# Kernel tuning notes

Hardware: AMD Instinct MI355X
Metric: run time of the kernel (lower is better)

Reference implementation:

```python
import jax, jax.numpy as jnp
import numpy as np

MARGIN = 0.5  # hardcoded in the torch __init__ regardless of the margin arg
P_IDS, K_PER_ID, K_PER_MOD = 32, 8, 4
B, C = P_IDS * K_PER_ID, 1024


def setup_inputs() -> dict:
    key = jax.random.key(0)
    inputs = jax.random.normal(key, (B, C), dtype=jnp.float32)
    # Standard cross-modal ReID sampler: P identities, K instances each,
    # first K/2 from modality 0, last K/2 from modality 1. This guarantees the
    # boolean-mask reshape in the original code is well-formed (M per row).
    targets = jnp.repeat(jnp.arange(P_IDS, dtype=jnp.int32), K_PER_ID)
    subs = jnp.tile(jnp.repeat(jnp.arange(2, dtype=jnp.int32), K_PER_MOD), P_IDS)
    return {"inputs": inputs, "targets": targets, "subs": subs, "m_count": K_PER_MOD}


def _loss(inputs, targets, subs, m_count):
    b, c = inputs.shape
    # Mask construction uses detached inputs in the original (clone().detach()).
    xs = jax.lax.stop_gradient(inputs)
    diff = jnp.abs(xs[:, None, :] - xs[None, :, :])                     # (B,B,C)
    identity_mask = targets[:, None] == targets[None, :]                # (B,B)
    modality_mask = subs[:, None] == subs[None, :]                      # (B,B)
    combined = identity_mask & modality_mask                            # (B,B)

    # diff[combined].reshape(B, M, C): every row has exactly m_count trues;
    # stable argsort recovers the selected column indices in ascending order,
    # matching torch's row-major boolean-mask gather.
    order = jnp.argsort(jnp.where(combined, 0, 1), axis=1)              # stable
    idx = order[:, :m_count]                                            # (B,M)
    modality_diff = jnp.take_along_axis(diff, idx[:, :, None], axis=1)  # (B,M,C)

    mean_md = modality_diff.mean(-1, keepdims=True)                     # (B,M,1)
    m_counts = (modality_diff < mean_md * MARGIN).sum(1)                # (B,C) int
    # mdm[i,j,c] = m_counts[i,c] * m_counts[j,c]  (detached float mask)
    mdm = (m_counts[:, None, :] * m_counts[None, :, :]).astype(inputs.dtype)  # (B,B,C)

    mean_d = diff.mean(-1, keepdims=True)                               # (B,B,1)
    idm = (diff < mean_d * MARGIN).astype(inputs.dtype)                 # (B,B,C)

    # Gradient-carrying pairwise differences (vectorized form of the B-loop).
    d = inputs[:, None, :] - inputs[None, :, :]                         # (B,B,C)
    mod_dist = jnp.sqrt(jnp.maximum(((d * mdm) ** 2).sum(-1), 1e-12))   # (B,B)
    id_dist = jnp.sqrt(jnp.maximum(((d * idm) ** 2).sum(-1), 1e-12))    # (B,B)
    id_dist = jnp.where(identity_mask, jnp.inf, id_dist)                # drop same-id

    per_row = jnp.maximum(mod_dist.max(axis=1) * 10.0 - id_dist.min(axis=1), 0.0)
    return per_row.mean()


def reference(inputs, targets, subs, m_count):
    return _loss(inputs, targets, subs, m_count)
```

## Files before the change

### kernel.cpp

```cpp
#include <hip/hip_runtime.h>
#include <math.h>

#define BB 256
#define CC 1024
#define CC4 (CC/4)
#define MARGIN 0.5f
#define NTILE 64
#define JPT 4
#define NP  128

__global__ __launch_bounds__(64) void mcsq_kernel(
    const float* __restrict__ x, const int* __restrict__ targets,
    const int* __restrict__ subs, const int* __restrict__ m_count_p,
    float* __restrict__ mcsq, float* __restrict__ acc,
    unsigned int* __restrict__ cnt_g)
{
    const int i = blockIdx.x;
    const int lane = threadIdx.x;
    if (i == 0 && lane == 0) { *acc = 0.f; *cnt_g = 0u; }
    const int ti = targets[i], si = subs[i];
    int mc = *m_count_p;
    if (mc > 8) mc = 8;

    unsigned long long masks[4];
    #pragma unroll
    for (int q = 0; q < 4; ++q) {
        const int j = q * 64 + lane;
        masks[q] = __ballot(targets[j] == ti && subs[j] == si);
    }
    int idx[8];
    int cnt = 0;
    for (int q = 0; q < 4 && cnt < mc; ++q) {
        unsigned long long m = masks[q];
        while (m && cnt < mc) {
            const int b = __ffsll(m) - 1;
            idx[cnt++] = q * 64 + b;
            m &= m - 1;
        }
    }
    for (int q = 0; q < 4 && cnt < mc; ++q) {
        unsigned long long m = ~masks[q];
        while (m && cnt < mc) {
            const int b = __ffsll(m) - 1;
            idx[cnt++] = q * 64 + b;
            m &= m - 1;
        }
    }

    const float4* x4 = (const float4*)x;
    float4 xi[4];
    #pragma unroll
    for (int t = 0; t < 4; ++t) xi[t] = x4[(long)i * CC4 + lane + 64 * t];

    float4 c4[4];
    #pragma unroll
    for (int t = 0; t < 4; ++t) c4[t] = make_float4(0.f, 0.f, 0.f, 0.f);

    for (int k = 0; k < cnt; ++k) {
        float4 ad[4];
        float s = 0.f;
        #pragma unroll
        for (int t = 0; t < 4; ++t) {
            const float4 xj = x4[(long)idx[k] * CC4 + lane + 64 * t];
            ad[t].x = fabsf(xi[t].x - xj.x);
            ad[t].y = fabsf(xi[t].y - xj.y);
            ad[t].z = fabsf(xi[t].z - xj.z);
            ad[t].w = fabsf(xi[t].w - xj.w);
            s += ad[t].x + ad[t].y + ad[t].z + ad[t].w;
        }
        #pragma unroll
        for (int off = 32; off > 0; off >>= 1) s += __shfl_xor(s, off, 64);
        const float thr = s * (MARGIN / CC);
        #pragma unroll
        for (int t = 0; t < 4; ++t) {
            c4[t].x += (ad[t].x < thr) ? 1.f : 0.f;
            c4[t].y += (ad[t].y < thr) ? 1.f : 0.f;
            c4[t].z += (ad[t].z < thr) ? 1.f : 0.f;
            c4[t].w += (ad[t].w < thr) ? 1.f : 0.f;
        }
    }
    float4* m4 = (float4*)mcsq;
    #pragma unroll
    for (int t = 0; t < 4; ++t) {
        float4 o;
        o.x = c4[t].x * c4[t].x;
        o.y = c4[t].y * c4[t].y;
        o.z = c4[t].z * c4[t].z;
        o.w = c4[t].w * c4[t].w;
        m4[(long)i * CC4 + lane + 64 * t] = o;
    }
}

__global__ __launch_bounds__(256) void pair_kernel(
    const float* __restrict__ x, const float* __restrict__ mcsq,
    const int* __restrict__ targets,
    float* __restrict__ pmax, float* __restrict__ pmin,
    float* __restrict__ pmaxT, float* __restrict__ pminT)
{
    const int tid  = threadIdx.x;
    const int lane = tid & 63;
    const int gw   = blockIdx.x * 4 + (tid >> 6);

    int h = (int)((129.0f - sqrtf(16641.0f - 4.0f * (float)gw)) * 0.5f);
    if (h > 63) h = 63;
    if (h < 0) h = 0;
    while (h > 0 && (129 * h - h * h) > gw) --h;
    while ((129 * (h + 1) - (h + 1) * (h + 1)) <= gw) ++h;
    const int r     = gw - (129 * h - h * h);
    const int cnt_h = 64 - h;
    const int p     = 2 * h + r / cnt_h;
    const int jt    = h + r % cnt_h;

    const int i0 = 2 * p, i1 = 2 * p + 1;

    const float4* x4 = (const float4*)x;
    const float4* m4 = (const float4*)mcsq;

    float4 xi0[4], xi1[4], mi0[4], mi1[4];
    #pragma unroll
    for (int t = 0; t < 4; ++t) {
        const int c4 = lane + 64 * t;
        xi0[t] = x4[(long)i0 * CC4 + c4];
        xi1[t] = x4[(long)i1 * CC4 + c4];
        mi0[t] = m4[(long)i0 * CC4 + c4];
        mi1[t] = m4[(long)i1 * CC4 + c4];
    }
    const int t0 = targets[i0], t1 = targets[i1];

    float max0 = 0.f, max1 = 0.f;
    float min0 = INFINITY, min1 = INFINITY;

    #pragma unroll
    for (int half = 0; half < 2; ++half) {
        const int ja = jt * JPT + 2 * half;
        const int jb = ja + 1;
        const int tja = targets[ja], tjb = targets[jb];

        float4 xa[4], xb[4];
        #pragma unroll
        for (int t = 0; t < 4; ++t) {
            const int c4 = lane + 64 * t;
            xa[t] = x4[(long)ja * CC4 + c4];
            xb[t] = x4[(long)jb * CC4 + c4];
        }

        float s0a = 0.f, s1a = 0.f, s0b = 0.f, s1b = 0.f;
        #pragma unroll
        for (int t = 0; t < 4; ++t) {
            s0a += fabsf(xi0[t].x - xa[t].x) + fabsf(xi0[t].y - xa[t].y)
                 + fabsf(xi0[t].z - xa[t].z) + fabsf(xi0[t].w - xa[t].w);
            s1a += fabsf(xi1[t].x - xa[t].x) + fabsf(xi1[t].y - xa[t].y)
                 + fabsf(xi1[t].z - xa[t].z) + fabsf(xi1[t].w - xa[t].w);
            s0b += fabsf(xi0[t].x - xb[t].x) + fabsf(xi0[t].y - xb[t].y)
                 + fabsf(xi0[t].z - xb[t].z) + fabsf(xi0[t].w - xb[t].w);
            s1b += fabsf(xi1[t].x - xb[t].x) + fabsf(xi1[t].y - xb[t].y)
                 + fabsf(xi1[t].z - xb[t].z) + fabsf(xi1[t].w - xb[t].w);
        }

        float4 maa[4], mab[4];
        #pragma unroll
        for (int t = 0; t < 4; ++t) {
            const int c4 = lane + 64 * t;
            maa[t] = m4[(long)ja * CC4 + c4];
            mab[t] = m4[(long)jb * CC4 + c4];
        }

        #pragma unroll
        for (int off = 32; off > 0; off >>= 1) {
            s0a += __shfl_xor(s0a, off, 64);
            s1a += __shfl_xor(s1a, off, 64);
            s0b += __shfl_xor(s0b, off, 64);
            s1b += __shfl_xor(s1b, off, 64);
        }
        const float thr0a = s0a * (MARGIN / CC);
        const float thr1a = s1a * (MARGIN / CC);
        const float thr0b = s0b * (MARGIN / CC);
        const float thr1b = s1b * (MARGIN / CC);

        float ids0a = 0.f, ids1a = 0.f, md0a = 0.f, md1a = 0.f;
        float ids0b = 0.f, ids1b = 0.f, md0b = 0.f, md1b = 0.f;
        #pragma unroll
        for (int t = 0; t < 4; ++t) {
            #pragma unroll
            for (int u = 0; u < 4; ++u) {
                const float x0v  = (&xi0[t].x)[u];
                const float x1v  = (&xi1[t].x)[u];
                const float m0v  = (&mi0[t].x)[u];
                const float m1v  = (&mi1[t].x)[u];
                const float xav  = (&xa[t].x)[u];
                const float mav  = (&maa[t].x)[u];
                const float xbv  = (&xb[t].x)[u];
                const float mbv  = (&mab[t].x)[u];

                const float d0a = x0v - xav;
                const float q0a = d0a * d0a;
                ids0a += (fabsf(d0a) < thr0a) ? q0a : 0.f;
                md0a  += q0a * m0v * mav;
                const float d1a = x1v - xav;
                const float q1a = d1a * d1a;
                ids1a += (fabsf(d1a) < thr1a) ? q1a : 0.f;
                md1a  += q1a * m1v * mav;

                const float d0b = x0v - xbv;
                const float q0b = d0b * d0b;
                ids0b += (fabsf(d0b) < thr0b) ? q0b : 0.f;
                md0b  += q0b * m0v * mbv;
                const float d1b = x1v - xbv;
                const float q1b = d1b * d1b;
                ids1b += (fabsf(d1b) < thr1b) ? q1b : 0.f;
                md1b  += q1b * m1v * mbv;
            }
        }

        #pragma unroll
        for (int off = 32; off > 0; off >>= 1) {
            ids0a += __shfl_xor(ids0a, off, 64);
            ids1a += __shfl_xor(ids1a, off, 64);
            md0a  += __shfl_xor(md0a,  off, 64);
            md1a  += __shfl_xor(md1a,  off, 64);
            ids0b += __shfl_xor(ids0b, off, 64);
            ids1b += __shfl_xor(ids1b, off, 64);
            md0b  += __shfl_xor(md0b,  off, 64);
            md1b  += __shfl_xor(md1b,  off, 64);
        }

        const float mod0a = sqrtf(fmaxf(md0a, 1e-12f));
        const float mod1a = sqrtf(fmaxf(md1a, 1e-12f));
        const float mod0b = sqrtf(fmaxf(md0b, 1e-12f));
        const float mod1b = sqrtf(fmaxf(md1b, 1e-12f));
        max0 = fmaxf(fmaxf(max0, mod0a), mod0b);
        max1 = fmaxf(fmaxf(max1, mod1a), mod1b);

        float id0a = sqrtf(fmaxf(ids0a, 1e-12f));
        float id1a = sqrtf(fmaxf(ids1a, 1e-12f));
        float id0b = sqrtf(fmaxf(ids0b, 1e-12f));
        float id1b = sqrtf(fmaxf(ids1b, 1e-12f));

        if (tja != t0) min0 = fminf(min0, id0a); else id0a = INFINITY;
        if (tja != t1) min1 = fminf(min1, id1a); else id1a = INFINITY;
        if (tjb != t0) min0 = fminf(min0, id0b); else id0b = INFINITY;
        if (tjb != t1) min1 = fminf(min1, id1b); else id1b = INFINITY;

        if (lane == 0) {
            pmaxT[ja * NP + p] = fmaxf(mod0a, mod1a);
            pminT[ja * NP + p] = fminf(id0a, id1a);
            pmaxT[jb * NP + p] = fmaxf(mod0b, mod1b);
            pminT[jb * NP + p] = fminf(id0b, id1b);
        }
    }

    if (lane == 0) {
        pmax[i0 * NTILE + jt] = max0;
        pmax[i1 * NTILE + jt] = max1;
        pmin[i0 * NTILE + jt] = min0;
        pmin[i1 * NTILE + jt] = min1;
    }
}

__global__ __launch_bounds__(64) void final_kernel(
    const float* __restrict__ pmax, const float* __restrict__ pmin,
    const float* __restrict__ pmaxT, const float* __restrict__ pminT,
    float* __restrict__ acc, unsigned int* __restrict__ cnt_g,
    float* __restrict__ out)
{
    const int i = blockIdx.x;
    const int lane = threadIdx.x;
    const int s = i >> 2;
    float mx = 0.f, mn = INFINITY;
    const int t = s + lane;
    if (t < NTILE) {
        mx = fmaxf(mx, pmax[i * NTILE + t]);
        mn = fminf(mn, pmin[i * NTILE + t]);
    }
    const int pv = 2 * s + 2;
    if (lane < pv) {
        mx = fmaxf(mx, pmaxT[i * NP + lane]);
        mn = fminf(mn, pminT[i * NP + lane]);
    }
    if (lane + 64 < pv) {
        mx = fmaxf(mx, pmaxT[i * NP + lane + 64]);
        mn = fminf(mn, pminT[i * NP + lane + 64]);
    }
    #pragma unroll
    for (int off = 32; off > 0; off >>= 1) {
        mx = fmaxf(mx, __shfl_xor(mx, off, 64));
        mn = fminf(mn, __shfl_xor(mn, off, 64));
    }
    if (lane == 0) {
        const float per = fmaxf(mx * 10.f - mn, 0.f);
        atomicAdd(acc, per * (1.0f / BB));
        __threadfence();
        const unsigned int old = atomicAdd(cnt_g, 1u);
        if (old == BB - 1) {
            __threadfence();
            out[0] = atomicAdd(acc, 0.0f);
        }
    }
}

extern "C" void kernel_launch(void* const* d_in, const int* in_sizes, int n_in,
                              void* d_out, int out_size, void* d_ws, size_t ws_size,
                              hipStream_t stream)
{
    const float* x       = (const float*)d_in[0];
    const int*   targets = (const int*)d_in[1];
    const int*   subs    = (const int*)d_in[2];
    const int*   m_count = (const int*)d_in[3];
    float* out  = (float*)d_out;

    float* mcsq  = (float*)d_ws;
    float* pmax  = mcsq  + (long)BB * CC;
    float* pmin  = pmax  + BB * NTILE;
    float* pmaxT = pmin  + BB * NTILE;
    float* pminT = pmaxT + BB * NP;
    float* acc   = pminT + BB * NP;
    unsigned int* cnt_g = (unsigned int*)(acc + 1);

    mcsq_kernel <<<BB,   64, 0, stream>>>(x, targets, subs, m_count, mcsq, acc, cnt_g);
    pair_kernel <<<1040, 256, 0, stream>>>(x, mcsq, targets, pmax, pmin, pmaxT, pminT);
    final_kernel<<<BB,   64, 0, stream>>>(pmax, pmin, pmaxT, pminT, acc, cnt_g, out);
}
```

Baseline: 93.74 us.

## Share j-tile rows across block warps via LDS in pair kernel

Remaps the triangular work decomposition so that all four warps in a block process the same j-tile with different i-pairs. The block stages the four j rows of x and mcsq once into shared memory, and each warp reads them from there instead of from global memory. This is meant to cut redundant global loads of the j operands by a factor of four. In exchange it adds a 32KB LDS allocation and a __syncthreads, which may limit occupancy, and some padding warps in the triangular mapping exit without doing work.

```diff
diff --git a/kernel.cpp b/kernel.cpp
--- a/kernel.cpp
+++ b/kernel.cpp
@@ -99,19 +99,24 @@
 {
     const int tid  = threadIdx.x;
     const int lane = tid & 63;
-    const int gw   = blockIdx.x * 4 + (tid >> 6);
-
-    int h = (int)((129.0f - sqrtf(16641.0f - 4.0f * (float)gw)) * 0.5f);
-    if (h > 63) h = 63;
-    if (h < 0) h = 0;
-    while (h > 0 && (129 * h - h * h) > gw) --h;
-    while ((129 * (h + 1) - (h + 1) * (h + 1)) <= gw) ++h;
-    const int r     = gw - (129 * h - h * h);
-    const int cnt_h = 64 - h;
-    const int p     = 2 * h + r / cnt_h;
-    const int jt    = h + r % cnt_h;
-
-    const int i0 = 2 * p, i1 = 2 * p + 1;
+    const int w    = tid >> 6;
+    const int b    = blockIdx.x;
+
+    int k = (int)((sqrtf(4.0f * (float)b + 1.0f) - 1.0f) * 0.5f);
+    if (k < 0) k = 0;
+    while (k > 0 && k * (k + 1) > b) --k;
+    while ((k + 1) * (k + 2) <= b) ++k;
+    const int off = b - k * (k + 1);
+    const int jt  = (off < k + 1) ? 2 * k : 2 * k + 1;
+    const int pg  = (off < k + 1) ? off : off - (k + 1);
+    const int p   = pg * 4 + w;
+    const bool valid = (p <= 2 * jt + 1);
+    const int pe  = valid ? p : 0;
+    const int i0  = 2 * pe, i1 = 2 * pe + 1;
+    const int j0  = jt * JPT;
+
+    __shared__ float lds[8192];
+    float4* lds4 = (float4*)lds;
 
     const float4* x4 = (const float4*)x;
     const float4* m4 = (const float4*)mcsq;
@@ -125,23 +130,40 @@
         mi0[t] = m4[(long)i0 * CC4 + c4];
         mi1[t] = m4[(long)i1 * CC4 + c4];
     }
+    float4 st[8];
+    #pragma unroll
+    for (int q = 0; q < 4; ++q) {
+        st[q]     = x4[(long)(j0 + q) * CC4 + tid];
+        st[4 + q] = m4[(long)(j0 + q) * CC4 + tid];
+    }
+    #pragma unroll
+    for (int q = 0; q < 8; ++q) lds4[q * 256 + tid] = st[q];
+    __syncthreads();
+
+    if (!valid) return;
+
     const int t0 = targets[i0], t1 = targets[i1];
+
+    const float4* lx = lds4;
+    const float4* lm = lds4 + 1024;
 
     float max0 = 0.f, max1 = 0.f;
     float min0 = INFINITY, min1 = INFINITY;
 
     #pragma unroll
     for (int half = 0; half < 2; ++half) {
-        const int ja = jt * JPT + 2 * half;
-        const int jb = ja + 1;
+        const int jal = 2 * half;
+        const int jbl = jal + 1;
+        const int ja  = j0 + jal;
+        const int jb  = j0 + jbl;
         const int tja = targets[ja], tjb = targets[jb];
 
         float4 xa[4], xb[4];
         #pragma unroll
         for (int t = 0; t < 4; ++t) {
             const int c4 = lane + 64 * t;
-            xa[t] = x4[(long)ja * CC4 + c4];
-            xb[t] = x4[(long)jb * CC4 + c4];
+            xa[t] = lx[jal * 256 + c4];
+            xb[t] = lx[jbl * 256 + c4];
         }
 
         float s0a = 0.f, s1a = 0.f, s0b = 0.f, s1b = 0.f;
@@ -161,16 +183,16 @@
         #pragma unroll
         for (int t = 0; t < 4; ++t) {
             const int c4 = lane + 64 * t;
-            maa[t] = m4[(long)ja * CC4 + c4];
-            mab[t] = m4[(long)jb * CC4 + c4];
-        }
-
-        #pragma unroll
-        for (int off = 32; off > 0; off >>= 1) {
-            s0a += __shfl_xor(s0a, off, 64);
-            s1a += __shfl_xor(s1a, off, 64);
-            s0b += __shfl_xor(s0b, off, 64);
-            s1b += __shfl_xor(s1b, off, 64);
+            maa[t] = lm[jal * 256 + c4];
+            mab[t] = lm[jbl * 256 + c4];
+        }
+
+        #pragma unroll
+        for (int off2 = 32; off2 > 0; off2 >>= 1) {
+            s0a += __shfl_xor(s0a, off2, 64);
+            s1a += __shfl_xor(s1a, off2, 64);
+            s0b += __shfl_xor(s0b, off2, 64);
+            s1b += __shfl_xor(s1b, off2, 64);
         }
         const float thr0a = s0a * (MARGIN / CC);
         const float thr1a = s1a * (MARGIN / CC);
@@ -213,15 +235,15 @@
         }
 
         #pragma unroll
-        for (int off = 32; off > 0; off >>= 1) {
-            ids0a += __shfl_xor(ids0a, off, 64);
-            ids1a += __shfl_xor(ids1a, off, 64);
-            md0a  += __shfl_xor(md0a,  off, 64);
-            md1a  += __shfl_xor(md1a,  off, 64);
-            ids0b += __shfl_xor(ids0b, off, 64);
-            ids1b += __shfl_xor(ids1b, off, 64);
-            md0b  += __shfl_xor(md0b,  off, 64);
-            md1b  += __shfl_xor(md1b,  off, 64);
+        for (int off2 = 32; off2 > 0; off2 >>= 1) {
+            ids0a += __shfl_xor(ids0a, off2, 64);
+            ids1a += __shfl_xor(ids1a, off2, 64);
+            md0a  += __shfl_xor(md0a,  off2, 64);
+            md1a  += __shfl_xor(md1a,  off2, 64);
+            ids0b += __shfl_xor(ids0b, off2, 64);
+            ids1b += __shfl_xor(ids1b, off2, 64);
+            md0b  += __shfl_xor(md0b,  off2, 64);
+            md1b  += __shfl_xor(md1b,  off2, 64);
         }
 
         const float mod0a = sqrtf(fmaxf(md0a, 1e-12f));
@@ -317,6 +339,6 @@
     unsigned int* cnt_g = (unsigned int*)(acc + 1);
 
     mcsq_kernel <<<BB,   64, 0, stream>>>(x, targets, subs, m_count, mcsq, acc, cnt_g);
-    pair_kernel <<<1040, 256, 0, stream>>>(x, mcsq, targets, pmax, pmin, pmaxT, pminT);
+    pair_kernel <<<1056, 256, 0, stream>>>(x, mcsq, targets, pmax, pmin, pmaxT, pminT);
     final_kernel<<<BB,   64, 0, stream>>>(pmax, pmin, pmaxT, pminT, acc, cnt_g, out);
 }
```

Measured after the change: 95.29 us. No clear change (+1.7%).
